# Optimization experiments

Measured on AMD Instinct MI355X. Metric: run time of the kernel, lower is better.

## Reference

```python
import jax, jax.numpy as jnp
import numpy as np

SHAPE = 64
K = 8
HID = 512
OUT = K + 2 * K * SHAPE + 2 * SHAPE  # 1160
B, T = 32, 2048


def setup_inputs() -> dict:
    key = jax.random.key(0)
    ks = jax.random.split(key, 4)
    x = jax.random.normal(ks[0], (B, T, SHAPE), dtype=jnp.float32)
    W1 = jax.random.normal(ks[1], (SHAPE, HID), dtype=jnp.float32) / np.sqrt(SHAPE)
    b1 = jnp.zeros((HID,), dtype=jnp.float32)
    W2 = jax.random.normal(ks[2], (HID, HID), dtype=jnp.float32) / np.sqrt(HID)
    b2 = jnp.zeros((HID,), dtype=jnp.float32)
    W3 = jax.random.normal(ks[3], (HID, OUT), dtype=jnp.float32) / np.sqrt(HID) * 0.1
    b3 = jnp.zeros((OUT,), dtype=jnp.float32)
    return {"x": x, "W1": W1, "b1": b1, "W2": W2, "b2": b2, "W3": W3, "b3": b3}


def _coupling_forward(x, W1, b1, W2, b2, W3, b3):
    # coupling mask over feature dim: first half conditions the second half
    mask = jnp.zeros((SHAPE,), dtype=x.dtype).at[:SHAPE // 2].set(1.0)  # [D]
    x_ = x * mask  # [B,T,D]

    # conditioner MLP
    h = jax.nn.relu(x_ @ W1 + b1)
    h = jax.nn.relu(h @ W2 + b2)
    params = h @ W3 + b3  # [B,T,OUT]

    logscales = params[..., :SHAPE]
    biases = params[..., SHAPE:2 * SHAPE]
    mdn = params[..., 2 * SHAPE:]
    logits = mdn[..., :K]                                   # [B,T,K]
    mu = mdn[..., K:K + K * SHAPE].reshape(*x.shape[:2], K, SHAPE)
    logstd = mdn[..., K + K * SHAPE:].reshape(*x.shape[:2], K, SHAPE)

    # --- MixtureCDFFlow.flow ---
    weights = jax.nn.softmax(logits, axis=-1)[..., None]    # [B,T,K,1]
    std = jnp.exp(logstd)
    u = (x[:, :, None, :] - mu) / std                       # [B,T,K,D]
    cdf = 0.5 * (1.0 + jax.lax.erf(u / np.sqrt(2.0)))
    z = jnp.sum(cdf * weights, axis=2)                      # [B,T,D]
    pdf = jnp.exp(-0.5 * u * u) / (std * np.sqrt(2.0 * np.pi))
    logd_mix = jnp.log(jnp.sum(pdf * weights, axis=2))      # [B,T,D]

    # --- Inverse(Sigmoid).flow == Sigmoid.invert ---
    xs = -jnp.log(1.0 / z - 1.0)
    logd_sig = -jnp.log(z) - jnp.log(1.0 - z)

    # --- ElemwiseAffine.flow ---
    out = xs * jnp.exp(logscales) + biases
    log_det = logd_mix + logd_sig + logscales

    x_out = (1.0 - mask) * out + x_
    log_det = log_det * (1.0 - mask)
    return x_out, log_det


def reference(x, W1, b1, W2, b2, W3, b3):
    return _coupling_forward(x, W1, b1, W2, b2, W3, b3)
```

## Files before the change

kernel.cpp:

```cpp
#include <hip/hip_runtime.h>

typedef short short8 __attribute__((ext_vector_type(8)));
typedef float f32x4 __attribute__((ext_vector_type(4)));

#define NROWS 65536
#define NCOMPACT 640

__device__ __forceinline__ short f2bf(float f) {
  union { float f; unsigned u; } c; c.f = f;
  unsigned r = (c.u + 0x7fffu + ((c.u >> 16) & 1u)) >> 16;
  return (short)r;
}

__device__ __forceinline__ float fastrcp(float a) {
  float r; asm("v_rcp_f32 %0, %1" : "=v"(r) : "v"(a)); return r;
}

__device__ __forceinline__ int w3col(int n) {
  if (n < 32)  return 32 + n;
  if (n < 64)  return 96 + (n - 32);
  if (n < 72)  return 128 + (n - 64);
  if (n < 96)  return -1;
  if (n < 352) { int q = n - 96;  return 168 + (q >> 5) * 64 + (q & 31); }
  if (n < 608) { int q = n - 352; return 680 + (q >> 5) * 64 + (q & 31); }
  return -1;
}

__global__ __launch_bounds__(256) void prep_w_kernel(
    const float* __restrict__ W1, const float* __restrict__ W2,
    const float* __restrict__ W3, const float* __restrict__ b3,
    short* __restrict__ w1t, short* __restrict__ w2t,
    short* __restrict__ w3t, float* __restrict__ b3c) {
  const int NW1 = 512 * 32, NW2 = 512 * 512, NW3 = NCOMPACT * 512;
  int t = blockIdx.x * 256 + threadIdx.x;
  if (t < NW1) {
    int n = t >> 5, k = t & 31;
    w1t[t] = f2bf(W1[k * 512 + n]);
  } else if (t < NW1 + NW2) {
    int i = t - NW1; int n = i >> 9, k = i & 511;
    w2t[i] = f2bf(W2[k * 512 + n]);
  } else if (t < NW1 + NW2 + NW3) {
    int i = t - NW1 - NW2; int n = i >> 9, k = i & 511;
    int c = w3col(n);
    w3t[i] = (c >= 0) ? f2bf(W3[(size_t)k * 1160 + c]) : (short)0;
  } else if (t < NW1 + NW2 + NW3 + NCOMPACT) {
    int n = t - NW1 - NW2 - NW3;
    int c = w3col(n);
    b3c[n] = (c >= 0) ? b3[c] : 0.0f;
  }
}

#define ASTR 40
__global__ __launch_bounds__(256, 4) void g12_kernel(
    const float* __restrict__ x,
    const short* __restrict__ w1t,
    const float* __restrict__ b1,
    const short* __restrict__ w2t,
    const float* __restrict__ b2,
    short* __restrict__ h2) {
  __shared__ __attribute__((aligned(16))) short As[128 * ASTR];
  __shared__ __attribute__((aligned(16))) short Bs[2][128 * 32];
  __shared__ __attribute__((aligned(16))) short W1b[2][32 * 32];
  const int tid = threadIdx.x;
  const int cpx = gridDim.x >> 3;
  const int s = blockIdx.x;
  const int w = (s & 7) * cpx + (s >> 3);
  const int m0 = (w >> 2) * 128, n0 = (w & 3) * 128;
  const int lane = tid & 63, wid = tid >> 6;
  const int wm = (wid >> 1) * 64, wn = (wid & 1) * 64;
  const int lr = lane & 15, hi = lane >> 4, lk = hi * 8;

  short8 xcf[2];
#pragma unroll
  for (int mi = 0; mi < 2; ++mi) {
    int row = m0 + wid * 32 + mi * 16 + lr;
    const float* xs = x + (size_t)row * 64 + lk;
    f32x4 v0 = *(const f32x4*)xs;
    f32x4 v1 = *(const f32x4*)(xs + 4);
    short8 v;
#pragma unroll
    for (int i = 0; i < 4; ++i) { v[i] = f2bf(v0[i]); v[4 + i] = f2bf(v1[i]); }
    xcf[mi] = v;
  }

  auto STAGE_B = [&](int buf, int kt) {
#pragma unroll
    for (int base = wid * 64; base < 512; base += 256) {
      int c = base + lane;
      int row = c >> 2;
      int skb = ((c & 3) ^ ((row >> 1) & 3)) << 4;
      const char* g = (const char*)(w2t + (size_t)(n0 + row) * 512 + kt) + skb;
      __builtin_amdgcn_global_load_lds(
          (const __attribute__((address_space(1))) void*)g,
          (__attribute__((address_space(3))) void*)((char*)Bs[buf] + base * 16),
          16, 0, 0);
    }
  };
  auto STAGE_W1 = [&](int buf, int kt) {
    if (wid < 2) {
      int c = wid * 64 + lane;
      int row = c >> 2;
      int skb = ((c & 3) ^ ((row >> 1) & 3)) << 4;
      const char* g = (const char*)(w1t + (size_t)(kt + row) * 32) + skb;
      __builtin_amdgcn_global_load_lds(
          (const __attribute__((address_space(1))) void*)g,
          (__attribute__((address_space(3))) void*)((char*)W1b[buf] + wid * 1024),
          16, 0, 0);
    }
  };

  auto H1STEP = [&](int buf, int kt) {
    const short* Wb = W1b[buf];
    short8 wf[2];
#pragma unroll
    for (int ni = 0; ni < 2; ++ni) {
      int row = ni * 16 + lr;
      wf[ni] = *(const short8*)(&Wb[row * 32 + (lk ^ (((row >> 1) & 3) << 3))]);
    }
    f32x4 a1[2][2] = {};
#pragma unroll
    for (int mi = 0; mi < 2; ++mi)
#pragma unroll
      for (int ni = 0; ni < 2; ++ni)
        a1[mi][ni] = __builtin_amdgcn_mfma_f32_16x16x32_bf16(
            xcf[mi], wf[ni], a1[mi][ni], 0, 0, 0);
#pragma unroll
    for (int ni = 0; ni < 2; ++ni) {
      int acol = ni * 16 + lr;
      float bv = b1[kt + acol];
#pragma unroll
      for (int mi = 0; mi < 2; ++mi)
#pragma unroll
        for (int j = 0; j < 4; ++j) {
          int arow = wid * 32 + mi * 16 + hi * 4 + j;
          As[arow * ASTR + acol] = f2bf(fmaxf(a1[mi][ni][j] + bv, 0.0f));
        }
    }
  };

  f32x4 acc[4][4] = {};
  auto COMPUTE = [&](int buf) {
    short8 af[4], bf_[4];
#pragma unroll
    for (int mi = 0; mi < 4; ++mi) {
      int row = wm + mi * 16 + lr;
      af[mi] = *(const short8*)(&As[row * ASTR + lk]);
    }
#pragma unroll
    for (int ni = 0; ni < 4; ++ni) {
      int row = wn + ni * 16 + lr;
      bf_[ni] = *(const short8*)(&Bs[buf][row * 32 + (lk ^ (((row >> 1) & 3) << 3))]);
    }
#pragma unroll
    for (int mi = 0; mi < 4; ++mi)
#pragma unroll
      for (int ni = 0; ni < 4; ++ni)
        acc[mi][ni] = __builtin_amdgcn_mfma_f32_16x16x32_bf16(
            af[mi], bf_[ni], acc[mi][ni], 0, 0, 0);
  };

  STAGE_B(0, 0); STAGE_W1(0, 0);
  __syncthreads();
  for (int t = 0; t < 16; ++t) {
    int pb = t & 1;
    if (t < 15) { STAGE_B(pb ^ 1, (t + 1) * 32); STAGE_W1(pb ^ 1, (t + 1) * 32); }
    H1STEP(pb, t * 32);
    __syncthreads();
    COMPUTE(pb);
    __syncthreads();
  }

#pragma unroll
  for (int ni = 0; ni < 4; ++ni) {
    int col = n0 + wn + ni * 16 + lr;
    float bv = b2[col];
#pragma unroll
    for (int mi = 0; mi < 4; ++mi) {
#pragma unroll
      for (int j = 0; j < 4; ++j) {
        int row = m0 + wm + mi * 16 + hi * 4 + j;
        h2[(size_t)row * 512 + col] = f2bf(fmaxf(acc[mi][ni][j] + bv, 0.0f));
      }
    }
  }
}

#define PSTR 644
#define BUF1 49152
__global__ __launch_bounds__(1024, 4) void gemm3_fused_kernel(
    const short* __restrict__ A,
    const short* __restrict__ Bw,
    const float* __restrict__ b3c,
    const float* __restrict__ x,
    float* __restrict__ out) {
  __shared__ __attribute__((aligned(16))) char lds[98304];
  const int tid = threadIdx.x;
  const int m0 = blockIdx.x * 128;
  const int lane = tid & 63, wid = tid >> 6;
  const int wr = wid >> 2, wc = wid & 3;
  const int lr = lane & 15, hi = lane >> 4, lk = hi * 8;

  f32x4 acc[2][10] = {};

  auto STAGE = [&](int bo, int kt) {
#pragma unroll
    for (int base = wid * 64; base < 3072; base += 1024) {
      int c = base + lane;
      char* dst = lds + bo + (size_t)base * 16;
      if (base < 512) {
        int row = c >> 2;
        int skb = ((c & 3) ^ ((row >> 1) & 3)) << 4;
        const char* ga = (const char*)(A + (size_t)(m0 + row) * 512 + kt) + skb;
        __builtin_amdgcn_global_load_lds(
            (const __attribute__((address_space(1))) void*)ga,
            (__attribute__((address_space(3))) void*)dst, 16, 0, 0);
      } else {
        int q = c - 512;
        int row = q >> 2;
        int skb = ((q & 3) ^ ((row >> 1) & 3)) << 4;
        const char* gb = (const char*)(Bw + (size_t)row * 512 + kt) + skb;
        __builtin_amdgcn_global_load_lds(
            (const __attribute__((address_space(1))) void*)gb,
            (__attribute__((address_space(3))) void*)dst, 16, 0, 0);
      }
    }
  };

  auto COMPUTE = [&](int bo) {
    const short* As = (const short*)(lds + bo);
    const short* Bs = (const short*)(lds + bo + 8192);
    short8 af[2];
#pragma unroll
    for (int mi = 0; mi < 2; ++mi) {
      int row = wr * 32 + mi * 16 + lr;
      int k = lk ^ (((row >> 1) & 3) << 3);
      af[mi] = *(const short8*)(&As[row * 32 + k]);
    }
#pragma unroll
    for (int ni = 0; ni < 10; ++ni) {
      int brow = wc * 160 + ni * 16 + lr;
      int k = lk ^ (((brow >> 1) & 3) << 3);
      short8 bf_ = *(const short8*)(&Bs[brow * 32 + k]);
      acc[0][ni] = __builtin_amdgcn_mfma_f32_16x16x32_bf16(af[0], bf_, acc[0][ni], 0, 0, 0);
      acc[1][ni] = __builtin_amdgcn_mfma_f32_16x16x32_bf16(af[1], bf_, acc[1][ni], 0, 0, 0);
    }
  };

  STAGE(0, 0);
  __syncthreads();
  for (int t = 0; t < 16; t += 2) {
    STAGE(BUF1, (t + 1) * 32);
    COMPUTE(0);
    __syncthreads();
    if (t < 14) STAGE(0, (t + 2) * 32);
    COMPUTE(BUF1);
    __syncthreads();
  }

  float* plds = (float*)lds;
  float* xo  = out;
  float* ldo = out + (size_t)NROWS * 64;
#pragma unroll
  for (int p = 0; p < 4; ++p) {
    if (p) __syncthreads();
    if (wr == p) {
#pragma unroll
      for (int mi = 0; mi < 2; ++mi) {
#pragma unroll
        for (int ni = 0; ni < 10; ++ni) {
          int col = wc * 160 + ni * 16 + lr;
          float bv = b3c[col];
#pragma unroll
          for (int j = 0; j < 4; ++j)
            plds[(mi * 16 + hi * 4 + j) * PSTR + col] = acc[mi][ni][j] + bv;
        }
      }
    }
    __syncthreads();
    {
      int rl = tid >> 5, j = tid & 31;
      const float* p_ = plds + rl * PSTR;
      int grow = m0 + p * 32 + rl;

      float lg[8];
#pragma unroll
      for (int k = 0; k < 8; ++k) lg[k] = p_[64 + k];
      float mx = lg[0];
#pragma unroll
      for (int k = 1; k < 8; ++k) mx = fmaxf(mx, lg[k]);
      float wgt[8], wsum = 0.0f;
#pragma unroll
      for (int k = 0; k < 8; ++k) { wgt[k] = __expf(lg[k] - mx); wsum += wgt[k]; }

      float xd = x[(size_t)grow * 64 + 32 + j];
      float zs = 0.0f, ps = 0.0f;
#pragma unroll
      for (int k = 0; k < 8; ++k) {
        float mu   = p_[96 + k * 32 + j];
        float lstd = p_[352 + k * 32 + j];
        float istd = __expf(-lstd);
        float u = (xd - mu) * istd;
        float x2 = 0.5f * u * u;
        float e  = __expf(-x2);
        ps += wgt[k] * e * istd;
        float ax = fabsf(u) * 0.70710678118654752f;
        float t_ = fastrcp(fmaf(0.5f, ax, 1.0f));
        float poly = -1.26551223f + t_*(1.00002368f + t_*(0.37409196f +
                     t_*(0.09678418f + t_*(-0.18628806f + t_*(0.27886807f +
                     t_*(-1.13520398f + t_*(1.48851587f + t_*(-0.82215223f +
                     t_*0.17087277f))))))));
        float erfc_half = 0.5f * t_ * __expf(poly - x2);
        float cdf = (u >= 0.0f) ? 1.0f - erfc_half : erfc_half;
        zs += wgt[k] * cdf;
      }
      float winv = fastrcp(wsum);
      float z  = zs * winv;
      float pm = ps * winv * 0.39894228040143268f;
      float logz = __logf(z), log1mz = __logf(1.0f - z);
      float ls = p_[j], bv = p_[32 + j];
      float outv = (logz - log1mz) * __expf(ls) + bv;
      float ld = __logf(pm) - logz - log1mz + ls;

      size_t base = (size_t)grow * 64;
      xo[base + j]       = x[base + j];
      xo[base + 32 + j]  = outv;
      ldo[base + j]      = 0.0f;
      ldo[base + 32 + j] = ld;
    }
  }
}

extern "C" void kernel_launch(void* const* d_in, const int* in_sizes, int n_in,
                              void* d_out, int out_size, void* d_ws, size_t ws_size,
                              hipStream_t stream) {
  const float* x  = (const float*)d_in[0];
  const float* W1 = (const float*)d_in[1];
  const float* b1 = (const float*)d_in[2];
  const float* W2 = (const float*)d_in[3];
  const float* b2 = (const float*)d_in[4];
  const float* W3 = (const float*)d_in[5];
  const float* b3 = (const float*)d_in[6];
  char* ws = (char*)d_ws;

  short* h2  = (short*)ws;
  short* w1t = (short*)(ws + 67108864);
  short* w2t = (short*)(ws + 67141632);
  short* w3t = (short*)(ws + 67665920);
  float* b3c = (float*)(ws + 68321280);
  float* out = (float*)d_out;

  {
    int total = 512 * 32 + 512 * 512 + NCOMPACT * 512 + NCOMPACT;
    prep_w_kernel<<<(total + 255) / 256, 256, 0, stream>>>(W1, W2, W3, b3, w1t, w2t, w3t, b3c);
  }
  g12_kernel<<<2048, 256, 0, stream>>>(x, w1t, b1, w2t, b2, h2);
  gemm3_fused_kernel<<<NROWS / 128, 1024, 0, stream>>>(h2, w3t, b3c, x, out);
}
```

Baseline: 133.4 us.

## Give each wave its own h1 rows to drop mid-loop block barrier

Changes the g12 warp tiling from a 2x2 grid of 64x64 tiles to four 32x128 row strips. Each wave computes the h1 rows it needs for GEMM2 and writes them to a private LDS scratch, so the shared As buffer and the block-wide barrier between H1 and GEMM2 go away. In exchange each wave re-reads all 8 B fragments per step (more LDS traffic for B) and needs a same-wave LDS write-then-read without an explicit wave barrier.

```diff
diff --git a/kernel.cpp b/kernel.cpp
--- a/kernel.cpp
+++ b/kernel.cpp
@@ -50,7 +50,7 @@
   }
 }
 
-#define ASTR 40
+#define SSTR 40
 __global__ __launch_bounds__(256, 4) void g12_kernel(
     const float* __restrict__ x,
     const short* __restrict__ w1t,
@@ -58,16 +58,15 @@
     const short* __restrict__ w2t,
     const float* __restrict__ b2,
     short* __restrict__ h2) {
-  __shared__ __attribute__((aligned(16))) short As[128 * ASTR];
   __shared__ __attribute__((aligned(16))) short Bs[2][128 * 32];
   __shared__ __attribute__((aligned(16))) short W1b[2][32 * 32];
+  __shared__ __attribute__((aligned(16))) short Sx[4][32 * SSTR];
   const int tid = threadIdx.x;
   const int cpx = gridDim.x >> 3;
   const int s = blockIdx.x;
   const int w = (s & 7) * cpx + (s >> 3);
   const int m0 = (w >> 2) * 128, n0 = (w & 3) * 128;
   const int lane = tid & 63, wid = tid >> 6;
-  const int wm = (wid >> 1) * 64, wn = (wid & 1) * 64;
   const int lr = lane & 15, hi = lane >> 4, lk = hi * 8;
 
   short8 xcf[2];
@@ -109,6 +108,7 @@
     }
   };
 
+  short8 af[2];
   auto H1STEP = [&](int buf, int kt) {
     const short* Wb = W1b[buf];
     short8 wf[2];
@@ -124,6 +124,7 @@
       for (int ni = 0; ni < 2; ++ni)
         a1[mi][ni] = __builtin_amdgcn_mfma_f32_16x16x32_bf16(
             xcf[mi], wf[ni], a1[mi][ni], 0, 0, 0);
+    short* S = Sx[wid];
 #pragma unroll
     for (int ni = 0; ni < 2; ++ni) {
       int acol = ni * 16 + lr;
@@ -131,32 +132,24 @@
 #pragma unroll
       for (int mi = 0; mi < 2; ++mi)
 #pragma unroll
-        for (int j = 0; j < 4; ++j) {
-          int arow = wid * 32 + mi * 16 + hi * 4 + j;
-          As[arow * ASTR + acol] = f2bf(fmaxf(a1[mi][ni][j] + bv, 0.0f));
-        }
-    }
-  };
-
-  f32x4 acc[4][4] = {};
+        for (int j = 0; j < 4; ++j)
+          S[(mi * 16 + hi * 4 + j) * SSTR + acol] =
+              f2bf(fmaxf(a1[mi][ni][j] + bv, 0.0f));
+    }
+#pragma unroll
+    for (int mi = 0; mi < 2; ++mi)
+      af[mi] = *(const short8*)(&S[(mi * 16 + lr) * SSTR + lk]);
+  };
+
+  f32x4 acc[2][8] = {};
   auto COMPUTE = [&](int buf) {
-    short8 af[4], bf_[4];
-#pragma unroll
-    for (int mi = 0; mi < 4; ++mi) {
-      int row = wm + mi * 16 + lr;
-      af[mi] = *(const short8*)(&As[row * ASTR + lk]);
-    }
-#pragma unroll
-    for (int ni = 0; ni < 4; ++ni) {
-      int row = wn + ni * 16 + lr;
-      bf_[ni] = *(const short8*)(&Bs[buf][row * 32 + (lk ^ (((row >> 1) & 3) << 3))]);
-    }
-#pragma unroll
-    for (int mi = 0; mi < 4; ++mi)
-#pragma unroll
-      for (int ni = 0; ni < 4; ++ni)
-        acc[mi][ni] = __builtin_amdgcn_mfma_f32_16x16x32_bf16(
-            af[mi], bf_[ni], acc[mi][ni], 0, 0, 0);
+#pragma unroll
+    for (int ni = 0; ni < 8; ++ni) {
+      int row = ni * 16 + lr;
+      short8 bf_ = *(const short8*)(&Bs[buf][row * 32 + (lk ^ (((row >> 1) & 3) << 3))]);
+      acc[0][ni] = __builtin_amdgcn_mfma_f32_16x16x32_bf16(af[0], bf_, acc[0][ni], 0, 0, 0);
+      acc[1][ni] = __builtin_amdgcn_mfma_f32_16x16x32_bf16(af[1], bf_, acc[1][ni], 0, 0, 0);
+    }
   };
 
   STAGE_B(0, 0); STAGE_W1(0, 0);
@@ -165,20 +158,19 @@
     int pb = t & 1;
     if (t < 15) { STAGE_B(pb ^ 1, (t + 1) * 32); STAGE_W1(pb ^ 1, (t + 1) * 32); }
     H1STEP(pb, t * 32);
-    __syncthreads();
     COMPUTE(pb);
     __syncthreads();
   }
 
 #pragma unroll
-  for (int ni = 0; ni < 4; ++ni) {
-    int col = n0 + wn + ni * 16 + lr;
+  for (int ni = 0; ni < 8; ++ni) {
+    int col = n0 + ni * 16 + lr;
     float bv = b2[col];
 #pragma unroll
-    for (int mi = 0; mi < 4; ++mi) {
+    for (int mi = 0; mi < 2; ++mi) {
 #pragma unroll
       for (int j = 0; j < 4; ++j) {
-        int row = m0 + wm + mi * 16 + hi * 4 + j;
+        int row = m0 + wid * 32 + mi * 16 + hi * 4 + j;
         h2[(size_t)row * 512 + col] = f2bf(fmaxf(acc[mi][ni][j] + bv, 0.0f));
       }
     }
```

Measured after the change: 133.6 us. Within noise of the previous version (+0.1%).

## Halve LDS in fused GEMM3 kernel by single-buffering and 16-row epilogue chunks

Applied to the files above, without the earlier changes.

Shrinks the shared-memory allocation of the fused third GEMM kernel from two staging buffers to one, so the K loop now loads a tile, syncs, computes and syncs again with no prefetch overlap. The epilogue is split into eight 16-row passes instead of four 32-row passes, so the parameter scratch fits in the smaller buffer, and only half the threads do the per-element flow math in each pass. The aim is to fit more blocks per CU by cutting LDS use, but it gives up the overlap of global loads with MFMA work and adds more barriers in the epilogue.

```diff
diff --git a/kernel.cpp b/kernel.cpp
--- a/kernel.cpp
+++ b/kernel.cpp
@@ -186,14 +186,13 @@
 }
 
 #define PSTR 644
-#define BUF1 49152
 __global__ __launch_bounds__(1024, 4) void gemm3_fused_kernel(
     const short* __restrict__ A,
     const short* __restrict__ Bw,
     const float* __restrict__ b3c,
     const float* __restrict__ x,
     float* __restrict__ out) {
-  __shared__ __attribute__((aligned(16))) char lds[98304];
+  __shared__ __attribute__((aligned(16))) char lds[49152];
   const int tid = threadIdx.x;
   const int m0 = blockIdx.x * 128;
   const int lane = tid & 63, wid = tid >> 6;
@@ -202,11 +201,11 @@
 
   f32x4 acc[2][10] = {};
 
-  auto STAGE = [&](int bo, int kt) {
+  auto STAGE = [&](int kt) {
 #pragma unroll
     for (int base = wid * 64; base < 3072; base += 1024) {
       int c = base + lane;
-      char* dst = lds + bo + (size_t)base * 16;
+      char* dst = lds + (size_t)base * 16;
       if (base < 512) {
         int row = c >> 2;
         int skb = ((c & 3) ^ ((row >> 1) & 3)) << 4;
@@ -226,9 +225,9 @@
     }
   };
 
-  auto COMPUTE = [&](int bo) {
-    const short* As = (const short*)(lds + bo);
-    const short* Bs = (const short*)(lds + bo + 8192);
+  auto COMPUTE = [&]() {
+    const short* As = (const short*)lds;
+    const short* Bs = (const short*)(lds + 8192);
     short8 af[2];
 #pragma unroll
     for (int mi = 0; mi < 2; ++mi) {
@@ -246,14 +245,10 @@
     }
   };
 
-  STAGE(0, 0);
-  __syncthreads();
-  for (int t = 0; t < 16; t += 2) {
-    STAGE(BUF1, (t + 1) * 32);
-    COMPUTE(0);
-    __syncthreads();
-    if (t < 14) STAGE(0, (t + 2) * 32);
-    COMPUTE(BUF1);
+  for (int t = 0; t < 16; ++t) {
+    STAGE(t * 32);
+    __syncthreads();
+    COMPUTE();
     __syncthreads();
   }
 
@@ -261,26 +256,24 @@
   float* xo  = out;
   float* ldo = out + (size_t)NROWS * 64;
 #pragma unroll
-  for (int p = 0; p < 4; ++p) {
+  for (int p = 0; p < 8; ++p) {
     if (p) __syncthreads();
-    if (wr == p) {
-#pragma unroll
-      for (int mi = 0; mi < 2; ++mi) {
-#pragma unroll
-        for (int ni = 0; ni < 10; ++ni) {
-          int col = wc * 160 + ni * 16 + lr;
-          float bv = b3c[col];
-#pragma unroll
-          for (int j = 0; j < 4; ++j)
-            plds[(mi * 16 + hi * 4 + j) * PSTR + col] = acc[mi][ni][j] + bv;
-        }
+    if (wr == (p >> 1)) {
+      int mi = p & 1;
+#pragma unroll
+      for (int ni = 0; ni < 10; ++ni) {
+        int col = wc * 160 + ni * 16 + lr;
+        float bv = b3c[col];
+#pragma unroll
+        for (int j = 0; j < 4; ++j)
+          plds[(hi * 4 + j) * PSTR + col] = acc[mi][ni][j] + bv;
       }
     }
     __syncthreads();
-    {
+    if (tid < 512) {
       int rl = tid >> 5, j = tid & 31;
       const float* p_ = plds + rl * PSTR;
-      int grow = m0 + p * 32 + rl;
+      int grow = m0 + p * 16 + rl;
 
       float lg[8];
 #pragma unroll
```

Measured after the change: 157.4 us. 1.18x slower.
